# Optimization experiments

Hardware: AMD Instinct MI355X
Metric: run time of the kernel (lower is better)

The kernel has to match this reference:

```python
import jax, jax.numpy as jnp
import numpy as np

R_W, T_W, P_W = 1.0, 1.0, 1.0
B, N_COLS = 4096, 6144  # N_COLS = 3 * n_vecs


def setup_inputs() -> dict:
    key = jax.random.key(0)
    k1, k2 = jax.random.split(key)
    preds = jax.random.normal(k1, (B, N_COLS), dtype=jnp.float32)  # logits
    targs = jax.random.uniform(k2, (B, N_COLS), dtype=jnp.float32)  # in [0,1]
    return {"preds": preds, "targs": targs}


def reference(preds, targs):
    # logits=True path: apply sigmoid to preds
    p = jax.nn.sigmoid(preds)
    b, n_vecs = p.shape[0], p.shape[1] // 3

    # NOTE: faithful to original torch code, which slices along the BATCH dim
    # (preds[0::3] == preds[0::3, :]), i.e. every 3rd row.
    r_loss = R_W * jnp.mean(jnp.abs(p[0::3] - targs[0::3]))
    theta_loss = T_W * jnp.mean(jnp.abs(p[1::3] - targs[1::3]))

    # phi: original loops b in range(B), v in range(2, B, 3) (bug: B, not 3*n_vecs),
    # with min over wraparound distances {|p-t|, |p-(t+1)|, |p-(t-1)|} per scalar.
    v_idx = jnp.arange(2, b, 3)              # columns 2,5,... < B
    pp = p[:, v_idx]                          # [B, n_v]
    tt = targs[:, v_idx]                      # [B, n_v]
    d = jnp.abs(pp - tt)
    d = jnp.minimum(d, jnp.abs(pp - (tt + 1.0)))
    d = jnp.minimum(d, jnp.abs(pp - (tt - 1.0)))
    phi_loss = P_W * jnp.sum(d) / (b * n_vecs)

    loss = r_loss + theta_loss + phi_loss
    return jnp.stack([loss, r_loss, theta_loss, phi_loss])
```

## Files before the change

### kernel.cpp

```cpp
#include <hip/hip_runtime.h>

#define NROWS 4096
#define NCOLS 6144
#define TPB   256
#define CHUNKS 6


__global__ void __launch_bounds__(256)
spherical_main(const float4* __restrict__ preds,
               const float4* __restrict__ targs,
               float* __restrict__ pr, float* __restrict__ pt,
               float* __restrict__ pp) {
    const int row = blockIdx.x;
    const int tid = threadIdx.x;
    const float4* prow = preds + row * (NCOLS / 4);
    const float4* trow = targs + row * (NCOLS / 4);

    float4 p[CHUNKS], t[CHUNKS];
#pragma unroll
    for (int k = 0; k < CHUNKS; ++k) p[k] = prow[tid + TPB * k];
#pragma unroll
    for (int k = 0; k < CHUNKS; ++k) t[k] = trow[tid + TPB * k];
    asm volatile("" :
        "+v"(p[0].x),"+v"(p[0].y),"+v"(p[0].z),"+v"(p[0].w),
        "+v"(p[1].x),"+v"(p[1].y),"+v"(p[1].z),"+v"(p[1].w),
        "+v"(p[2].x),"+v"(p[2].y),"+v"(p[2].z),"+v"(p[2].w),
        "+v"(p[3].x),"+v"(p[3].y),"+v"(p[3].z),"+v"(p[3].w),
        "+v"(p[4].x),"+v"(p[4].y),"+v"(p[4].z),"+v"(p[4].w),
        "+v"(p[5].x),"+v"(p[5].y),"+v"(p[5].z),"+v"(p[5].w));
    asm volatile("" :
        "+v"(t[0].x),"+v"(t[0].y),"+v"(t[0].z),"+v"(t[0].w),
        "+v"(t[1].x),"+v"(t[1].y),"+v"(t[1].z),"+v"(t[1].w),
        "+v"(t[2].x),"+v"(t[2].y),"+v"(t[2].z),"+v"(t[2].w),
        "+v"(t[3].x),"+v"(t[3].y),"+v"(t[3].z),"+v"(t[3].w),
        "+v"(t[4].x),"+v"(t[4].y),"+v"(t[4].z),"+v"(t[4].w),
        "+v"(t[5].x),"+v"(t[5].y),"+v"(t[5].z),"+v"(t[5].w));

    const int tidm3 = tid % 3;
    float asum = 0.f, psum = 0.f;
#pragma unroll
    for (int k = 0; k < CHUNKS; ++k) {
        const float ps[4] = {p[k].x, p[k].y, p[k].z, p[k].w};
        const float ts[4] = {t[k].x, t[k].y, t[k].z, t[k].w};
#pragma unroll
        for (int j = 0; j < 4; ++j) {
            const float e = __expf(-ps[j]);
            const float s = __builtin_amdgcn_rcpf(1.0f + e);
            const float x = s - ts[j];
            const float a = fabsf(x);
            asum += a;
            if (k < 4) {
                const float d = fminf(a, fminf(fabsf(x - 1.f), fabsf(x + 1.f)));
                const int want = ((2 - k - j) % 3 + 3) % 3;
                psum += (tidm3 == want) ? d : 0.f;
            }
        }
    }

#pragma unroll
    for (int off = 32; off > 0; off >>= 1) {
        asum += __shfl_down(asum, off);
        psum += __shfl_down(psum, off);
    }
    __shared__ float la[4], lp[4];
    const int wave = tid >> 6, lane = tid & 63;
    if (lane == 0) { la[wave] = asum; lp[wave] = psum; }
    __syncthreads();

    if (tid == 0) {
        const float ba = la[0] + la[1] + la[2] + la[3];
        const float bp = lp[0] + lp[1] + lp[2] + lp[3];
        const int rm = row % 3;
        pr[row] = (rm == 0) ? ba : 0.f;
        pt[row] = (rm == 1) ? ba : 0.f;
        pp[row] = bp;
    }
}

__global__ void __launch_bounds__(1024)
spherical_final(const float* __restrict__ pr, const float* __restrict__ pt,
                const float* __restrict__ pp, float* __restrict__ out) {
    const int tid = threadIdx.x;
    double sr = 0.0, st = 0.0, sp = 0.0;
    for (int i = tid; i < NROWS; i += 1024) {
        sr += (double)pr[i]; st += (double)pt[i]; sp += (double)pp[i];
    }
#pragma unroll
    for (int off = 32; off > 0; off >>= 1) {
        sr += __shfl_down(sr, off);
        st += __shfl_down(st, off);
        sp += __shfl_down(sp, off);
    }
    __shared__ double dr[16], dt[16], dp[16];
    const int wave = tid >> 6, lane = tid & 63;
    if (lane == 0) { dr[wave] = sr; dt[wave] = st; dp[wave] = sp; }
    __syncthreads();
    if (tid == 0) {
        double r = 0.0, t = 0.0, p = 0.0;
#pragma unroll
        for (int w = 0; w < 16; ++w) { r += dr[w]; t += dt[w]; p += dp[w]; }
        r /= 1366.0 * 6144.0;
        t /= 1365.0 * 6144.0;
        p /= 4096.0 * 2048.0;
        out[0] = (float)(r + t + p);
        out[1] = (float)r;
        out[2] = (float)t;
        out[3] = (float)p;
    }
}

extern "C" void kernel_launch(void* const* d_in, const int* in_sizes, int n_in,
                              void* d_out, int out_size, void* d_ws, size_t ws_size,
                              hipStream_t stream) {
    const float4* preds = (const float4*)d_in[0];
    const float4* targs = (const float4*)d_in[1];
    float* pr = (float*)d_ws;
    float* pt = pr + NROWS;
    float* pp = pt + NROWS;

    spherical_main<<<dim3(NROWS), dim3(TPB), 0, stream>>>(preds, targs, pr, pt, pp);
    spherical_final<<<dim3(1), dim3(1024), 0, stream>>>(pr, pt, pp, (float*)d_out);
}
```

Measured before the change: 38.06 us.

## Skip unused column chunks on phi-only rows and pipeline loads with waitcnt

Rows with index mod 3 == 2 contribute only to the phi term, which reads columns below 4096, so those rows now load just the first four chunks instead of six. That cuts global traffic by roughly a ninth. Loads are issued through inline asm and consumed chunk by chunk behind staged s_waitcnt, so computation overlaps memory latency. The wraparound distance is simplified to min(a, 1-a), which assumes |x| <= 1 (true because sigmoid and targets both lie in [0,1]). Hand-written waitcnt and asm loads are brittle if the compiler inserts other memory operations.

```diff
diff --git a/kernel.cpp b/kernel.cpp
--- a/kernel.cpp
+++ b/kernel.cpp
@@ -3,77 +3,88 @@
 #define NROWS 4096
 #define NCOLS 6144
 #define TPB   256
-#define CHUNKS 6
+
+typedef float f32x4 __attribute__((ext_vector_type(4)));
 
 
+#define GLOAD(dst, ptr) \
+    asm volatile("global_load_dwordx4 %0, %1, off" : "=v"(dst) : "v"(ptr))
+#define WAITV(N) do { \
+    asm volatile("s_waitcnt vmcnt(" #N ")"); \
+    __builtin_amdgcn_sched_barrier(0); } while (0)
+
+template<int K, int BKT>
+__device__ __forceinline__ void chunk(f32x4 p, f32x4 t, int tidm3,
+                                      float& asum, float& psum) {
+#pragma unroll
+    for (int j = 0; j < 4; ++j) {
+        const float e = __expf(-p[j]);
+        const float s = __builtin_amdgcn_rcpf(1.0f + e);
+        const float x = s - t[j];
+        const float a = fabsf(x);
+        if (BKT != 2) asum += a;
+        if (K < 4) {
+            const float d = fminf(a, 1.0f - a);
+            const int want = ((2 - K - j) % 3 + 3) % 3;
+            psum += (tidm3 == want) ? d : 0.0f;
+        }
+    }
+}
+
 __global__ void __launch_bounds__(256)
-spherical_main(const float4* __restrict__ preds,
-               const float4* __restrict__ targs,
+spherical_main(const f32x4* __restrict__ preds,
+               const f32x4* __restrict__ targs,
                float* __restrict__ pr, float* __restrict__ pt,
                float* __restrict__ pp) {
     const int row = blockIdx.x;
     const int tid = threadIdx.x;
-    const float4* prow = preds + row * (NCOLS / 4);
-    const float4* trow = targs + row * (NCOLS / 4);
+    const f32x4* pA = preds + (size_t)row * (NCOLS / 4) + tid;
+    const f32x4* tA = targs + (size_t)row * (NCOLS / 4) + tid;
+    const int tidm3 = tid % 3;
+    const int kind  = row % 3;
 
-    float4 p[CHUNKS], t[CHUNKS];
-#pragma unroll
-    for (int k = 0; k < CHUNKS; ++k) p[k] = prow[tid + TPB * k];
-#pragma unroll
-    for (int k = 0; k < CHUNKS; ++k) t[k] = trow[tid + TPB * k];
-    asm volatile("" :
-        "+v"(p[0].x),"+v"(p[0].y),"+v"(p[0].z),"+v"(p[0].w),
-        "+v"(p[1].x),"+v"(p[1].y),"+v"(p[1].z),"+v"(p[1].w),
-        "+v"(p[2].x),"+v"(p[2].y),"+v"(p[2].z),"+v"(p[2].w),
-        "+v"(p[3].x),"+v"(p[3].y),"+v"(p[3].z),"+v"(p[3].w),
-        "+v"(p[4].x),"+v"(p[4].y),"+v"(p[4].z),"+v"(p[4].w),
-        "+v"(p[5].x),"+v"(p[5].y),"+v"(p[5].z),"+v"(p[5].w));
-    asm volatile("" :
-        "+v"(t[0].x),"+v"(t[0].y),"+v"(t[0].z),"+v"(t[0].w),
-        "+v"(t[1].x),"+v"(t[1].y),"+v"(t[1].z),"+v"(t[1].w),
-        "+v"(t[2].x),"+v"(t[2].y),"+v"(t[2].z),"+v"(t[2].w),
-        "+v"(t[3].x),"+v"(t[3].y),"+v"(t[3].z),"+v"(t[3].w),
-        "+v"(t[4].x),"+v"(t[4].y),"+v"(t[4].z),"+v"(t[4].w),
-        "+v"(t[5].x),"+v"(t[5].y),"+v"(t[5].z),"+v"(t[5].w));
+    float asum = 0.f, ps = 0.f;
 
-    const int tidm3 = tid % 3;
-    float asum = 0.f, psum = 0.f;
-#pragma unroll
-    for (int k = 0; k < CHUNKS; ++k) {
-        const float ps[4] = {p[k].x, p[k].y, p[k].z, p[k].w};
-        const float ts[4] = {t[k].x, t[k].y, t[k].z, t[k].w};
-#pragma unroll
-        for (int j = 0; j < 4; ++j) {
-            const float e = __expf(-ps[j]);
-            const float s = __builtin_amdgcn_rcpf(1.0f + e);
-            const float x = s - ts[j];
-            const float a = fabsf(x);
-            asum += a;
-            if (k < 4) {
-                const float d = fminf(a, fminf(fabsf(x - 1.f), fabsf(x + 1.f)));
-                const int want = ((2 - k - j) % 3 + 3) % 3;
-                psum += (tidm3 == want) ? d : 0.f;
-            }
-        }
+    if (kind != 2) {
+        f32x4 P[6], T[6];
+        GLOAD(P[0], pA + 0*TPB); GLOAD(T[0], tA + 0*TPB);
+        GLOAD(P[1], pA + 1*TPB); GLOAD(T[1], tA + 1*TPB);
+        GLOAD(P[2], pA + 2*TPB); GLOAD(T[2], tA + 2*TPB);
+        GLOAD(P[3], pA + 3*TPB); GLOAD(T[3], tA + 3*TPB);
+        GLOAD(P[4], pA + 4*TPB); GLOAD(T[4], tA + 4*TPB);
+        GLOAD(P[5], pA + 5*TPB); GLOAD(T[5], tA + 5*TPB);
+        WAITV(10); chunk<0,0>(P[0], T[0], tidm3, asum, ps);
+        WAITV(8);  chunk<1,0>(P[1], T[1], tidm3, asum, ps);
+        WAITV(6);  chunk<2,0>(P[2], T[2], tidm3, asum, ps);
+        WAITV(4);  chunk<3,0>(P[3], T[3], tidm3, asum, ps);
+        WAITV(2);  chunk<4,0>(P[4], T[4], tidm3, asum, ps);
+        WAITV(0);  chunk<5,0>(P[5], T[5], tidm3, asum, ps);
+    } else {
+        f32x4 P[4], T[4];
+        GLOAD(P[0], pA + 0*TPB); GLOAD(T[0], tA + 0*TPB);
+        GLOAD(P[1], pA + 1*TPB); GLOAD(T[1], tA + 1*TPB);
+        GLOAD(P[2], pA + 2*TPB); GLOAD(T[2], tA + 2*TPB);
+        GLOAD(P[3], pA + 3*TPB); GLOAD(T[3], tA + 3*TPB);
+        WAITV(6);  chunk<0,2>(P[0], T[0], tidm3, asum, ps);
+        WAITV(4);  chunk<1,2>(P[1], T[1], tidm3, asum, ps);
+        WAITV(2);  chunk<2,2>(P[2], T[2], tidm3, asum, ps);
+        WAITV(0);  chunk<3,2>(P[3], T[3], tidm3, asum, ps);
     }
 
 #pragma unroll
     for (int off = 32; off > 0; off >>= 1) {
         asum += __shfl_down(asum, off);
-        psum += __shfl_down(psum, off);
+        ps   += __shfl_down(ps, off);
     }
     __shared__ float la[4], lp[4];
     const int wave = tid >> 6, lane = tid & 63;
-    if (lane == 0) { la[wave] = asum; lp[wave] = psum; }
+    if (lane == 0) { la[wave] = asum; lp[wave] = ps; }
     __syncthreads();
-
     if (tid == 0) {
         const float ba = la[0] + la[1] + la[2] + la[3];
-        const float bp = lp[0] + lp[1] + lp[2] + lp[3];
-        const int rm = row % 3;
-        pr[row] = (rm == 0) ? ba : 0.f;
-        pt[row] = (rm == 1) ? ba : 0.f;
-        pp[row] = bp;
+        pr[row] = (kind == 0) ? ba : 0.f;
+        pt[row] = (kind == 1) ? ba : 0.f;
+        pp[row] = lp[0] + lp[1] + lp[2] + lp[3];
     }
 }
 
@@ -112,8 +123,8 @@
 extern "C" void kernel_launch(void* const* d_in, const int* in_sizes, int n_in,
                               void* d_out, int out_size, void* d_ws, size_t ws_size,
                               hipStream_t stream) {
-    const float4* preds = (const float4*)d_in[0];
-    const float4* targs = (const float4*)d_in[1];
+    const f32x4* preds = (const f32x4*)d_in[0];
+    const f32x4* targs = (const f32x4*)d_in[1];
     float* pr = (float*)d_ws;
     float* pt = pr + NROWS;
     float* pp = pt + NROWS;
```

After: 34.74 us. -8.7%, faster.
